# Performance work log

Measured on AMD Instinct MI355X. Metric: run time of the kernel, lower is better.

The kernel has to match this reference:

```python
import jax, jax.numpy as jnp
import numpy as np

F_TOKENS = 1024
D_TOKEN = 64
HIDDEN = 128


def setup_inputs() -> dict:
    key = jax.random.key(0)
    k1, k2, k3, k4, k5 = jax.random.split(key, 5)
    node = jax.random.normal(k1, (F_TOKENS, D_TOKEN), dtype=jnp.float32)
    # nn.Linear default init scale ~ 1/sqrt(fan_in); keep simple scaled randn
    W1 = jax.random.normal(k2, (2 * D_TOKEN, HIDDEN), dtype=jnp.float32) / np.sqrt(2 * D_TOKEN)
    b1 = jax.random.normal(k3, (HIDDEN,), dtype=jnp.float32) * 0.01
    w2 = jax.random.normal(k4, (HIDDEN,), dtype=jnp.float32) / np.sqrt(HIDDEN)
    b2 = jax.random.normal(k5, (1,), dtype=jnp.float32) * 0.01
    return {"node": node, "W1": W1, "b1": b1, "w2": w2, "b2": b2}


def reference(node, W1, b1, w2, b2):
    # Original: pair[i,j] = concat(node[i], node[j]);
    # Linear(2d->h) on the concat splits exactly into two d->h matmuls,
    # so we avoid materializing the [F,F,2d] concat tensor (same math).
    d = node.shape[1]
    a = node @ W1[:d]          # [F, h] contribution of v_i
    b = node @ W1[d:]          # [F, h] contribution of v_j
    h = jax.nn.gelu(a[:, None, :] + b[None, :, :] + b1, approximate=False)  # [F, F, h]
    logits = h @ w2 + b2[0]    # [F, F]
    return jax.nn.softmax(logits, axis=-1)
```

## Files before the change

kernel.cpp:

```cpp
#include <hip/hip_runtime.h>
#include <math.h>

#define F 1024
#define D 64
#define H 128

__global__ __launch_bounds__(128) void prep_kernel(
    const float* __restrict__ node, const float* __restrict__ W1,
    const float* __restrict__ b1,
    float* __restrict__ A, float* __restrict__ Bt) {
  const int i = blockIdx.x;
  const int k = threadIdx.x;
  __shared__ float n[D];
  if (k < D) n[k] = node[i * D + k];
  __syncthreads();
  float a = b1[k];
  float b = 0.f;
#pragma unroll
  for (int r = 0; r < D; ++r) {
    const float nv = n[r];
    a = fmaf(nv, W1[r * H + k], a);
    b = fmaf(nv, W1[(D + r) * H + k], b);
  }
  A[i * H + k] = a;
  Bt[k * F + i] = b;
}

#define C1 (-2.3022082f)
#define C2 (-0.10294323f)

__global__ __launch_bounds__(512) void pair_kernel(
    const float* __restrict__ A, const float* __restrict__ Bt,
    const float* __restrict__ w2, float* __restrict__ out) {
  const int i = blockIdx.x;
  const int tid = threadIdx.x;

  __shared__ float2 sAW[H];
  __shared__ float redm[8];
  __shared__ float reds[8];

  if (tid < H) sAW[tid] = make_float2(A[i * H + tid], w2[tid]);
  __syncthreads();

  float acc0 = 0.f, acc1 = 0.f;

  const float2* bp = reinterpret_cast<const float2*>(Bt) + tid;
#pragma unroll 8
  for (int k = 0; k < H; ++k) {
    const float2 b2v = bp[k * (F / 2)];
    const float2 aw = sAW[k];
    {
      const float x = aw.x + b2v.x;
      const float arg = x * fmaf(C2, x * x, C1);
      const float r = __builtin_amdgcn_rcpf(1.f + __builtin_amdgcn_exp2f(arg));
      acc0 = fmaf(aw.y * x, r, acc0);
    }
    {
      const float x = aw.x + b2v.y;
      const float arg = x * fmaf(C2, x * x, C1);
      const float r = __builtin_amdgcn_rcpf(1.f + __builtin_amdgcn_exp2f(arg));
      acc1 = fmaf(aw.y * x, r, acc1);
    }
  }

  const int wave = tid >> 6;
  const int lane = tid & 63;

  float m = fmaxf(acc0, acc1);
#pragma unroll
  for (int off = 32; off >= 1; off >>= 1)
    m = fmaxf(m, __shfl_xor(m, off, 64));
  if (lane == 0) redm[wave] = m;
  __syncthreads();
#pragma unroll
  for (int w = 0; w < 8; ++w) m = fmaxf(m, redm[w]);

  acc0 = __expf(acc0 - m);
  acc1 = __expf(acc1 - m);
  float s = acc0 + acc1;
#pragma unroll
  for (int off = 32; off >= 1; off >>= 1)
    s += __shfl_xor(s, off, 64);
  if (lane == 0) reds[wave] = s;
  __syncthreads();
  s = 0.f;
#pragma unroll
  for (int w = 0; w < 8; ++w) s += reds[w];

  const float inv = __builtin_amdgcn_rcpf(s);
  float2 o;
  o.x = acc0 * inv;
  o.y = acc1 * inv;
  *reinterpret_cast<float2*>(out + (size_t)i * F + 2 * tid) = o;
}

extern "C" void kernel_launch(void* const* d_in, const int* in_sizes, int n_in,
                              void* d_out, int out_size, void* d_ws, size_t ws_size,
                              hipStream_t stream) {
  const float* node = (const float*)d_in[0];
  const float* W1   = (const float*)d_in[1];
  const float* b1   = (const float*)d_in[2];
  const float* w2   = (const float*)d_in[3];
  float* out = (float*)d_out;

  float* A  = (float*)d_ws;
  float* Bt = A + (size_t)F * H;

  prep_kernel<<<F, H, 0, stream>>>(node, W1, b1, A, Bt);
  pair_kernel<<<F, 512, 0, stream>>>(A, Bt, w2, out);
}
```

Before: 49.80 us.

## Tile pair kernel over 4 rows with register-cached B column and split softmax

The pair kernel now has each thread own one column j across 4 rows i. It keeps all 128 B values for that column in registers and uses packed v2f math for the GELU polynomial and the accumulation. This cuts repeated global loads of Bt per row and lets the compiler use packed FP32 ops. Softmax moves into a separate kernel that reads the logits back from the output buffer, which adds a launch and an extra read/write of the 4MB output. The 128-float register array risks high VGPR pressure at the requested occupancy.

After: 104.5 us. +109.7%, slower.

```diff
diff --git a/kernel.cpp b/kernel.cpp
--- a/kernel.cpp
+++ b/kernel.cpp
@@ -4,6 +4,8 @@
 #define F 1024
 #define D 64
 #define H 128
+
+typedef float v2f __attribute__((ext_vector_type(2)));
 
 __global__ __launch_bounds__(128) void prep_kernel(
     const float* __restrict__ node, const float* __restrict__ W1,
@@ -29,69 +31,116 @@
 #define C1 (-2.3022082f)
 #define C2 (-0.10294323f)
 
-__global__ __launch_bounds__(512) void pair_kernel(
+__global__ __launch_bounds__(256, 3) void pair_kernel(
     const float* __restrict__ A, const float* __restrict__ Bt,
     const float* __restrict__ w2, float* __restrict__ out) {
-  const int i = blockIdx.x;
   const int tid = threadIdx.x;
+  const int jpanel = blockIdx.x & 3;
+  const int rp = blockIdx.x >> 2;
+  const int j = jpanel * 256 + tid;
+  const int i0 = rp * 4;
 
-  __shared__ float2 sAW[H];
-  __shared__ float redm[8];
-  __shared__ float reds[8];
+  __shared__ float4 sA[H];
+  __shared__ float4 sC[H / 4];
 
-  if (tid < H) sAW[tid] = make_float2(A[i * H + tid], w2[tid]);
+  if (tid < H)
+    sA[tid] = make_float4(A[(i0 + 0) * H + tid], A[(i0 + 1) * H + tid],
+                          A[(i0 + 2) * H + tid], A[(i0 + 3) * H + tid]);
+  if (tid < H / 4)
+    sC[tid] = reinterpret_cast<const float4*>(w2)[tid];
+
+  float B[H];
+#pragma unroll
+  for (int k = 0; k < H; ++k) B[k] = Bt[(size_t)k * F + j];
   __syncthreads();
 
-  float acc0 = 0.f, acc1 = 0.f;
+  v2f acc01 = {0.f, 0.f};
+  v2f acc23 = {0.f, 0.f};
 
-  const float2* bp = reinterpret_cast<const float2*>(Bt) + tid;
-#pragma unroll 8
-  for (int k = 0; k < H; ++k) {
-    const float2 b2v = bp[k * (F / 2)];
-    const float2 aw = sAW[k];
-    {
-      const float x = aw.x + b2v.x;
-      const float arg = x * fmaf(C2, x * x, C1);
-      const float r = __builtin_amdgcn_rcpf(1.f + __builtin_amdgcn_exp2f(arg));
-      acc0 = fmaf(aw.y * x, r, acc0);
-    }
-    {
-      const float x = aw.x + b2v.y;
-      const float arg = x * fmaf(C2, x * x, C1);
-      const float r = __builtin_amdgcn_rcpf(1.f + __builtin_amdgcn_exp2f(arg));
-      acc1 = fmaf(aw.y * x, r, acc1);
+#pragma unroll
+  for (int k4 = 0; k4 < H / 4; ++k4) {
+    const float4 c4 = sC[k4];
+    const float cc[4] = {c4.x, c4.y, c4.z, c4.w};
+#pragma unroll
+    for (int t = 0; t < 4; ++t) {
+      const int k = k4 * 4 + t;
+      const float bk = B[k];
+      const float4 a4 = sA[k];
+      const float wk = cc[t];
+      {
+        v2f X = {a4.x + bk, a4.y + bk};
+        const v2f U = X * X;
+        const v2f P = __builtin_elementwise_fma((v2f)(C2), U, (v2f)(C1));
+        const v2f Arg = X * P;
+        v2f E;
+        E.x = __builtin_amdgcn_exp2f(Arg.x);
+        E.y = __builtin_amdgcn_exp2f(Arg.y);
+        const v2f Dn = 1.0f + E;
+        v2f R;
+        R.x = __builtin_amdgcn_rcpf(Dn.x);
+        R.y = __builtin_amdgcn_rcpf(Dn.y);
+        acc01 = __builtin_elementwise_fma(wk * X, R, acc01);
+      }
+      {
+        v2f X = {a4.z + bk, a4.w + bk};
+        const v2f U = X * X;
+        const v2f P = __builtin_elementwise_fma((v2f)(C2), U, (v2f)(C1));
+        const v2f Arg = X * P;
+        v2f E;
+        E.x = __builtin_amdgcn_exp2f(Arg.x);
+        E.y = __builtin_amdgcn_exp2f(Arg.y);
+        const v2f Dn = 1.0f + E;
+        v2f R;
+        R.x = __builtin_amdgcn_rcpf(Dn.x);
+        R.y = __builtin_amdgcn_rcpf(Dn.y);
+        acc23 = __builtin_elementwise_fma(wk * X, R, acc23);
+      }
     }
   }
 
+  out[(size_t)(i0 + 0) * F + j] = acc01.x;
+  out[(size_t)(i0 + 1) * F + j] = acc01.y;
+  out[(size_t)(i0 + 2) * F + j] = acc23.x;
+  out[(size_t)(i0 + 3) * F + j] = acc23.y;
+}
+
+__global__ __launch_bounds__(256) void softmax_kernel(float* __restrict__ L) {
+  const int i = blockIdx.x;
+  const int tid = threadIdx.x;
   const int wave = tid >> 6;
   const int lane = tid & 63;
+  __shared__ float redm[4];
+  __shared__ float reds[4];
 
-  float m = fmaxf(acc0, acc1);
+  float4* row = reinterpret_cast<float4*>(L + (size_t)i * F);
+  float4 v = row[tid];
+
+  float m = fmaxf(fmaxf(v.x, v.y), fmaxf(v.z, v.w));
 #pragma unroll
   for (int off = 32; off >= 1; off >>= 1)
     m = fmaxf(m, __shfl_xor(m, off, 64));
   if (lane == 0) redm[wave] = m;
   __syncthreads();
-#pragma unroll
-  for (int w = 0; w < 8; ++w) m = fmaxf(m, redm[w]);
+  m = fmaxf(fmaxf(redm[0], redm[1]), fmaxf(redm[2], redm[3]));
 
-  acc0 = __expf(acc0 - m);
-  acc1 = __expf(acc1 - m);
-  float s = acc0 + acc1;
+  v.x = __expf(v.x - m);
+  v.y = __expf(v.y - m);
+  v.z = __expf(v.z - m);
+  v.w = __expf(v.w - m);
+  float s = v.x + v.y + v.z + v.w;
 #pragma unroll
   for (int off = 32; off >= 1; off >>= 1)
     s += __shfl_xor(s, off, 64);
   if (lane == 0) reds[wave] = s;
   __syncthreads();
-  s = 0.f;
-#pragma unroll
-  for (int w = 0; w < 8; ++w) s += reds[w];
+  s = reds[0] + reds[1] + reds[2] + reds[3];
 
   const float inv = __builtin_amdgcn_rcpf(s);
-  float2 o;
-  o.x = acc0 * inv;
-  o.y = acc1 * inv;
-  *reinterpret_cast<float2*>(out + (size_t)i * F + 2 * tid) = o;
+  v.x *= inv;
+  v.y *= inv;
+  v.z *= inv;
+  v.w *= inv;
+  row[tid] = v;
 }
 
 extern "C" void kernel_launch(void* const* d_in, const int* in_sizes, int n_in,
@@ -107,5 +156,6 @@
   float* Bt = A + (size_t)F * H;
 
   prep_kernel<<<F, H, 0, stream>>>(node, W1, b1, A, Bt);
-  pair_kernel<<<F, 512, 0, stream>>>(A, Bt, w2, out);
+  pair_kernel<<<(F / 4) * 4, 256, 0, stream>>>(A, Bt, w2, out);
+  softmax_kernel<<<F, 256, 0, stream>>>(out);
 }
```
